# Kernel optimization log

Measured on AMD Instinct MI355X. Metric: run time of the kernel, lower is better.

The kernel has to match this reference:

```python
import jax, jax.numpy as jnp
import numpy as np

THRESHOLD = 1.0
SLOPE = 25.0  # snntorch surrogate.fast_sigmoid default slope
BETA = 0.9

@jax.custom_vjp
def spike_fn(x):
    # Heaviside forward, fast-sigmoid surrogate backward: g / (slope*|x| + 1)^2
    return (x > 0).astype(x.dtype)

def _spike_fwd(x):
    return spike_fn(x), x

def _spike_bwd(x, g):
    return (g / (SLOPE * jnp.abs(x) + 1.0) ** 2,)

spike_fn.defvjp(_spike_fwd, _spike_bwd)


def setup_inputs() -> dict:
    key = jax.random.key(0)
    k_x, k_w1, k_b1, k_w2, k_b2 = jax.random.split(key, 5)
    B, T, F, H, O = 128, 256, 2500, 128, 2
    x = jax.random.normal(k_x, (B, T, F), dtype=jnp.float32)
    # PyTorch Linear init: U(-1/sqrt(fan_in), 1/sqrt(fan_in))
    s1 = 1.0 / np.sqrt(F)
    s2 = 1.0 / np.sqrt(H)
    W1 = jax.random.uniform(k_w1, (H, F), jnp.float32, -s1, s1)
    b1 = jax.random.uniform(k_b1, (H,), jnp.float32, -s1, s1)
    W2 = jax.random.uniform(k_w2, (O, H), jnp.float32, -s2, s2)
    b2 = jax.random.uniform(k_b2, (O,), jnp.float32, -s2, s2)
    return {"x": x, "W1": W1, "b1": b1, "W2": W2, "b2": b2}


def reference(x, W1, b1, W2, b2):
    # Module transposes to [time, batch, feat] when shape[0] < shape[1]
    if x.ndim == 3 and x.shape[0] < x.shape[1]:
        x = jnp.swapaxes(x, 0, 1)  # [T, B, F]
    T, B = x.shape[0], x.shape[1]
    H, O = W1.shape[0], W2.shape[0]

    def lif(mem, cur):
        # snntorch Leaky, reset_mechanism='subtract'; reset spike is detached
        rst = jax.lax.stop_gradient(spike_fn(mem - THRESHOLD))
        mem = BETA * mem + cur - rst * THRESHOLD
        spk = spike_fn(mem - THRESHOLD)
        return spk, mem

    def step(carry, xt):
        mem1, mem2 = carry
        cur1 = xt @ W1.T + b1            # [B, H]
        spk1, mem1 = lif(mem1, cur1)
        cur2 = spk1 @ W2.T + b2          # [B, O]
        spk2, mem2 = lif(mem2, cur2)
        return (mem1, mem2), (spk2, mem2)

    mem1_0 = jnp.zeros((B, H), x.dtype)
    mem2_0 = jnp.zeros((B, O), x.dtype)
    _, (spk_rec, mem_rec) = jax.lax.scan(step, (mem1_0, mem2_0), x)
    return spk_rec, mem_rec  # each [T, B, O]
```

## Files before the change

kernel.cpp:

```cpp
#include <hip/hip_runtime.h>

#define T_STEPS 256
#define B_SZ    128
#define F_SZ    2500
#define H_SZ    128
#define O_SZ    2

__global__ __launch_bounds__(256) void k_transpose(const float* __restrict__ W1,
                                                   float* __restrict__ W1T) {
    int idx = blockIdx.x * 256 + threadIdx.x;
    if (idx >= F_SZ * H_SZ) return;
    int k = idx >> 7;
    int h = idx & 127;
    W1T[idx] = W1[h * F_SZ + k];
}

__global__ __launch_bounds__(256, 1) void k_gemm(const float* __restrict__ x,
                                                 const float* __restrict__ W1T,
                                                 const float* __restrict__ b1g,
                                                 double* __restrict__ cur1) {
    __shared__ float Alds[32 * 128];
    __shared__ float Blds[32 * 128];

    const int t    = blockIdx.x;
    const int tid  = threadIdx.x;
    const int lane = tid & 63;
    const int w    = tid >> 6;
    const int wm   = w >> 1;
    const int wn   = w & 1;
    const int li   = lane & 7;
    const int lj   = lane >> 3;

    const int ac = tid & 7;
    const int ar = tid >> 3;
    const int bn = tid & 31;
    const int bk = tid >> 5;

    float4 aV[4], bV[4];

    auto loadA = [&](int k0) {
        const int k = k0 + ac * 4;
        const bool ok = (k < F_SZ);
        #pragma unroll
        for (int i = 0; i < 4; ++i) {
            const int rr = ar + i * 32;
            if (ok) aV[i] = *(const float4*)(x + (size_t)(rr * T_STEPS + t) * F_SZ + k);
            else    aV[i] = make_float4(0.f, 0.f, 0.f, 0.f);
        }
    };
    auto loadB = [&](int k0) {
        #pragma unroll
        for (int i = 0; i < 4; ++i) {
            const int k = k0 + bk + i * 8;
            if (k < F_SZ) bV[i] = *(const float4*)(W1T + k * H_SZ + bn * 4);
            else          bV[i] = make_float4(0.f, 0.f, 0.f, 0.f);
        }
    };
    auto storeTiles = [&]() {
        #pragma unroll
        for (int i = 0; i < 4; ++i) {
            const int rr = ar + i * 32;
            Alds[(ac * 4 + 0) * 128 + rr] = aV[i].x;
            Alds[(ac * 4 + 1) * 128 + rr] = aV[i].y;
            Alds[(ac * 4 + 2) * 128 + rr] = aV[i].z;
            Alds[(ac * 4 + 3) * 128 + rr] = aV[i].w;
            *(float4*)(Blds + (bk + i * 8) * 128 + bn * 4) = bV[i];
        }
    };

    double acc[2][2][4][4];
    #pragma unroll
    for (int a = 0; a < 2; ++a)
        #pragma unroll
        for (int b = 0; b < 2; ++b)
            #pragma unroll
            for (int i = 0; i < 4; ++i)
                #pragma unroll
                for (int j = 0; j < 4; ++j)
                    acc[a][b][i][j] = 0.0;

    const int NSTEP = (F_SZ + 31) / 32;
    loadA(0);
    loadB(0);

    #pragma unroll 1
    for (int s = 0; s < NSTEP; ++s) {
        __syncthreads();
        storeTiles();
        if (s + 1 < NSTEP) { loadA((s + 1) * 32); loadB((s + 1) * 32); }
        __syncthreads();

        const float* Ab = Alds + wm * 64 + li * 4;
        const float* Bb = Blds + wn * 64 + lj * 4;
        #pragma unroll
        for (int k = 0; k < 32; ++k) {
            const float4 a0  = *(const float4*)(Ab + k * 128);
            const float4 a1  = *(const float4*)(Ab + k * 128 + 32);
            const float4 bb0 = *(const float4*)(Bb + k * 128);
            const float4 bb1 = *(const float4*)(Bb + k * 128 + 32);
            const double av[2][4] = {{a0.x, a0.y, a0.z, a0.w}, {a1.x, a1.y, a1.z, a1.w}};
            const double bv[2][4] = {{bb0.x, bb0.y, bb0.z, bb0.w}, {bb1.x, bb1.y, bb1.z, bb1.w}};
            #pragma unroll
            for (int rh = 0; rh < 2; ++rh)
                #pragma unroll
                for (int i = 0; i < 4; ++i)
                    #pragma unroll
                    for (int ch = 0; ch < 2; ++ch)
                        #pragma unroll
                        for (int j = 0; j < 4; ++j)
                            acc[rh][ch][i][j] = fma(av[rh][i], bv[ch][j], acc[rh][ch][i][j]);
        }
    }

    const float4 bias0 = *(const float4*)(b1g + wn * 64 + lj * 4);
    const float4 bias1 = *(const float4*)(b1g + wn * 64 + lj * 4 + 32);
    const double bias[2][4] = {{bias0.x, bias0.y, bias0.z, bias0.w},
                               {bias1.x, bias1.y, bias1.z, bias1.w}};
    #pragma unroll
    for (int rh = 0; rh < 2; ++rh) {
        #pragma unroll
        for (int i = 0; i < 4; ++i) {
            const int r = wm * 64 + li * 4 + rh * 32 + i;
            double* outp = cur1 + (size_t)(t * 128 + r) * 128 + wn * 64 + lj * 4;
            #pragma unroll
            for (int j = 0; j < 4; ++j) {
                outp[j]      = acc[rh][0][i][j] + bias[0][j];
                outp[j + 32] = acc[rh][1][i][j] + bias[1][j];
            }
        }
    }
}

__global__ __launch_bounds__(256) void k_lif1(const double* __restrict__ cur1,
                                              float* __restrict__ spk1) {
    const int tid = blockIdx.x * 256 + threadIdx.x;
    double mem = 0.0;
    #pragma unroll 4
    for (int t = 0; t < T_STEPS; ++t) {
        const double cur = cur1[t * 16384 + tid];
        const double rst = (mem > 1.0) ? 1.0 : 0.0;
        mem = 0.9 * mem + cur - rst;
        spk1[t * 16384 + tid] = (mem > 1.0) ? 1.0f : 0.0f;
    }
}

__global__ __launch_bounds__(256) void k_cur2(const float* __restrict__ spk1,
                                              const float* __restrict__ W2,
                                              const float* __restrict__ b2,
                                              double* __restrict__ cur2) {
    const int wave = (blockIdx.x * 256 + threadIdx.x) >> 6;
    const int lane = threadIdx.x & 63;
    const float2 s  = *(const float2*)(spk1 + (size_t)wave * 128 + lane * 2);
    const float2 w0 = *(const float2*)(W2 + lane * 2);
    const float2 w1 = *(const float2*)(W2 + 128 + lane * 2);
    double v0 = (double)s.x * (double)w0.x + (double)s.y * (double)w0.y;
    double v1 = (double)s.x * (double)w1.x + (double)s.y * (double)w1.y;
    #pragma unroll
    for (int off = 32; off >= 1; off >>= 1) {
        v0 += __shfl_down(v0, off);
        v1 += __shfl_down(v1, off);
    }
    if (lane == 0) {
        cur2[wave * 2 + 0] = v0 + (double)b2[0];
        cur2[wave * 2 + 1] = v1 + (double)b2[1];
    }
}

__global__ __launch_bounds__(256) void k_lif2(const double* __restrict__ cur2,
                                              float* __restrict__ out) {
    const int tid = threadIdx.x;
    double mem = 0.0;
    float* spk_out = out;
    float* mem_out = out + T_STEPS * B_SZ * O_SZ;
    #pragma unroll 4
    for (int t = 0; t < T_STEPS; ++t) {
        const double cur = cur2[t * 256 + tid];
        const double rst = (mem > 1.0) ? 1.0 : 0.0;
        mem = 0.9 * mem + cur - rst;
        spk_out[t * 256 + tid] = (mem > 1.0) ? 1.0f : 0.0f;
        mem_out[t * 256 + tid] = (float)mem;
    }
}

extern "C" void kernel_launch(void* const* d_in, const int* in_sizes, int n_in,
                              void* d_out, int out_size, void* d_ws, size_t ws_size,
                              hipStream_t stream) {
    const float* x  = (const float*)d_in[0];
    const float* W1 = (const float*)d_in[1];
    const float* b1 = (const float*)d_in[2];
    const float* W2 = (const float*)d_in[3];
    const float* b2 = (const float*)d_in[4];
    float* out = (float*)d_out;

    char* ws = (char*)d_ws;
    double* cur1 = (double*)ws;
    float*  spk1 = (float*)(ws + 33554432);
    float*  W1T  = (float*)(ws + 33554432 + 16777216);
    double* cur2 = (double*)(ws + 33554432 + 16777216 + 1280000);

    k_transpose<<<1250, 256, 0, stream>>>(W1, W1T);
    k_gemm<<<256, 256, 0, stream>>>(x, W1T, b1, cur1);
    k_lif1<<<64, 256, 0, stream>>>(cur1, spk1);
    k_cur2<<<8192, 256, 0, stream>>>(spk1, W2, b2, cur2);
    k_lif2<<<1, 256, 0, stream>>>(cur2, out);
}
```

Baseline: 923.1 us.

## Switch layer-1 GEMM to fp32 with split-K and double-precision fixup for near-threshold neurons

```diff
diff --git a/kernel.cpp b/kernel.cpp
--- a/kernel.cpp
+++ b/kernel.cpp
@@ -5,24 +5,36 @@
 #define F_SZ    2500
 #define H_SZ    128
 #define O_SZ    2
+#define KSPLIT0 1248
+#define FLAG_WINDOW 1.25e-4
+#define MAX_FLAGS 16384
 
 __global__ __launch_bounds__(256) void k_transpose(const float* __restrict__ W1,
-                                                   float* __restrict__ W1T) {
+                                                   float* __restrict__ W1T,
+                                                   int* __restrict__ flag_count) {
     int idx = blockIdx.x * 256 + threadIdx.x;
+    if (idx == 0) *flag_count = 0;
     if (idx >= F_SZ * H_SZ) return;
     int k = idx >> 7;
     int h = idx & 127;
     W1T[idx] = W1[h * F_SZ + k];
 }
 
-__global__ __launch_bounds__(256, 1) void k_gemm(const float* __restrict__ x,
+__global__ __launch_bounds__(256, 2) void k_gemm(const float* __restrict__ x,
                                                  const float* __restrict__ W1T,
-                                                 const float* __restrict__ b1g,
-                                                 double* __restrict__ cur1) {
-    __shared__ float Alds[32 * 128];
-    __shared__ float Blds[32 * 128];
-
-    const int t    = blockIdx.x;
+                                                 float* __restrict__ curA,
+                                                 float* __restrict__ curB) {
+    __shared__ float4 Alds4[128 * 8];
+    __shared__ float  Blds [32 * 128];
+
+    const int bid   = blockIdx.x;
+    const int t     = bid >> 1;
+    const int split = bid & 1;
+    const int k0    = split ? KSPLIT0 : 0;
+    const int kend  = split ? F_SZ : KSPLIT0;
+    const int NSTEP = split ? 40 : 39;
+    float* outP = split ? curB : curA;
+
     const int tid  = threadIdx.x;
     const int lane = tid & 63;
     const int w    = tid >> 6;
@@ -33,14 +45,15 @@
 
     const int ac = tid & 7;
     const int ar = tid >> 3;
+    const int aswz = ac ^ ((ar >> 2) & 7);
     const int bn = tid & 31;
     const int bk = tid >> 5;
 
     float4 aV[4], bV[4];
 
-    auto loadA = [&](int k0) {
-        const int k = k0 + ac * 4;
-        const bool ok = (k < F_SZ);
+    auto loadA = [&](int kb) {
+        const int k = kb + ac * 4;
+        const bool ok = (k < kend);
         #pragma unroll
         for (int i = 0; i < 4; ++i) {
             const int rr = ar + i * 32;
@@ -48,11 +61,11 @@
             else    aV[i] = make_float4(0.f, 0.f, 0.f, 0.f);
         }
     };
-    auto loadB = [&](int k0) {
+    auto loadB = [&](int kb) {
         #pragma unroll
         for (int i = 0; i < 4; ++i) {
-            const int k = k0 + bk + i * 8;
-            if (k < F_SZ) bV[i] = *(const float4*)(W1T + k * H_SZ + bn * 4);
+            const int k = kb + bk + i * 8;
+            if (k < kend) bV[i] = *(const float4*)(W1T + (size_t)k * H_SZ + bn * 4);
             else          bV[i] = make_float4(0.f, 0.f, 0.f, 0.f);
         }
     };
@@ -60,15 +73,12 @@
         #pragma unroll
         for (int i = 0; i < 4; ++i) {
             const int rr = ar + i * 32;
-            Alds[(ac * 4 + 0) * 128 + rr] = aV[i].x;
-            Alds[(ac * 4 + 1) * 128 + rr] = aV[i].y;
-            Alds[(ac * 4 + 2) * 128 + rr] = aV[i].z;
-            Alds[(ac * 4 + 3) * 128 + rr] = aV[i].w;
+            Alds4[rr * 8 + aswz] = aV[i];
             *(float4*)(Blds + (bk + i * 8) * 128 + bn * 4) = bV[i];
         }
     };
 
-    double acc[2][2][4][4];
+    float acc[2][2][4][4];
     #pragma unroll
     for (int a = 0; a < 2; ++a)
         #pragma unroll
@@ -77,70 +87,158 @@
             for (int i = 0; i < 4; ++i)
                 #pragma unroll
                 for (int j = 0; j < 4; ++j)
-                    acc[a][b][i][j] = 0.0;
-
-    const int NSTEP = (F_SZ + 31) / 32;
-    loadA(0);
-    loadB(0);
+                    acc[a][b][i][j] = 0.f;
+
+    int abase[8];
+    #pragma unroll
+    for (int rh = 0; rh < 2; ++rh)
+        #pragma unroll
+        for (int i = 0; i < 4; ++i)
+            abase[rh * 4 + i] = (wm * 64 + rh * 32 + li * 4 + i) * 8;
+
+    const float4* Blds4 = (const float4*)Blds;
+    const int bbase = wn * 16 + lj;
+
+    loadA(k0);
+    loadB(k0);
 
     #pragma unroll 1
     for (int s = 0; s < NSTEP; ++s) {
         __syncthreads();
         storeTiles();
-        if (s + 1 < NSTEP) { loadA((s + 1) * 32); loadB((s + 1) * 32); }
+        if (s + 1 < NSTEP) { loadA(k0 + (s + 1) * 32); loadB(k0 + (s + 1) * 32); }
         __syncthreads();
 
-        const float* Ab = Alds + wm * 64 + li * 4;
-        const float* Bb = Blds + wn * 64 + lj * 4;
-        #pragma unroll
-        for (int k = 0; k < 32; ++k) {
-            const float4 a0  = *(const float4*)(Ab + k * 128);
-            const float4 a1  = *(const float4*)(Ab + k * 128 + 32);
-            const float4 bb0 = *(const float4*)(Bb + k * 128);
-            const float4 bb1 = *(const float4*)(Bb + k * 128 + 32);
-            const double av[2][4] = {{a0.x, a0.y, a0.z, a0.w}, {a1.x, a1.y, a1.z, a1.w}};
-            const double bv[2][4] = {{bb0.x, bb0.y, bb0.z, bb0.w}, {bb1.x, bb1.y, bb1.z, bb1.w}};
-            #pragma unroll
-            for (int rh = 0; rh < 2; ++rh)
+        #pragma unroll
+        for (int kc = 0; kc < 8; ++kc) {
+            const int kcli = kc ^ li;
+            float4 av4[8];
+            #pragma unroll
+            for (int r = 0; r < 8; ++r) av4[r] = Alds4[abase[r] + kcli];
+
+            #pragma unroll
+            for (int dk = 0; dk < 4; ++dk) {
+                const float4 bv0 = Blds4[(kc * 4 + dk) * 32 + bbase];
+                const float4 bv1 = Blds4[(kc * 4 + dk) * 32 + bbase + 8];
+                const float bvf[2][4] = {{bv0.x, bv0.y, bv0.z, bv0.w},
+                                         {bv1.x, bv1.y, bv1.z, bv1.w}};
                 #pragma unroll
-                for (int i = 0; i < 4; ++i)
+                for (int rh = 0; rh < 2; ++rh)
                     #pragma unroll
-                    for (int ch = 0; ch < 2; ++ch)
+                    for (int i = 0; i < 4; ++i) {
+                        const float4 a4 = av4[rh * 4 + i];
+                        const float af = (dk == 0) ? a4.x : (dk == 1) ? a4.y : (dk == 2) ? a4.z : a4.w;
                         #pragma unroll
-                        for (int j = 0; j < 4; ++j)
-                            acc[rh][ch][i][j] = fma(av[rh][i], bv[ch][j], acc[rh][ch][i][j]);
-        }
-    }
-
-    const float4 bias0 = *(const float4*)(b1g + wn * 64 + lj * 4);
-    const float4 bias1 = *(const float4*)(b1g + wn * 64 + lj * 4 + 32);
-    const double bias[2][4] = {{bias0.x, bias0.y, bias0.z, bias0.w},
-                               {bias1.x, bias1.y, bias1.z, bias1.w}};
+                        for (int ch = 0; ch < 2; ++ch)
+                            #pragma unroll
+                            for (int j = 0; j < 4; ++j)
+                                acc[rh][ch][i][j] = fmaf(af, bvf[ch][j], acc[rh][ch][i][j]);
+                    }
+            }
+        }
+    }
+
     #pragma unroll
     for (int rh = 0; rh < 2; ++rh) {
         #pragma unroll
         for (int i = 0; i < 4; ++i) {
-            const int r = wm * 64 + li * 4 + rh * 32 + i;
-            double* outp = cur1 + (size_t)(t * 128 + r) * 128 + wn * 64 + lj * 4;
-            #pragma unroll
-            for (int j = 0; j < 4; ++j) {
-                outp[j]      = acc[rh][0][i][j] + bias[0][j];
-                outp[j + 32] = acc[rh][1][i][j] + bias[1][j];
-            }
-        }
-    }
-}
-
-__global__ __launch_bounds__(256) void k_lif1(const double* __restrict__ cur1,
-                                              float* __restrict__ spk1) {
-    const int tid = blockIdx.x * 256 + threadIdx.x;
+            const int r = wm * 64 + rh * 32 + li * 4 + i;
+            float* outp = outP + (size_t)(t * 128 + r) * 128 + wn * 64 + lj * 4;
+            *(float4*)(outp)      = make_float4(acc[rh][0][i][0], acc[rh][0][i][1],
+                                                acc[rh][0][i][2], acc[rh][0][i][3]);
+            *(float4*)(outp + 32) = make_float4(acc[rh][1][i][0], acc[rh][1][i][1],
+                                                acc[rh][1][i][2], acc[rh][1][i][3]);
+        }
+    }
+}
+
+__global__ __launch_bounds__(256) void k_lif1(const float* __restrict__ curA,
+                                              const float* __restrict__ curB,
+                                              const float* __restrict__ b1,
+                                              float* __restrict__ spk1,
+                                              int* __restrict__ flag_count,
+                                              int* __restrict__ flag_list) {
+    const int idx = blockIdx.x * 256 + threadIdx.x;
+    const double b1v = (double)b1[idx & 127];
     double mem = 0.0;
-    #pragma unroll 4
+    bool flagged = false;
+    #pragma unroll 8
     for (int t = 0; t < T_STEPS; ++t) {
-        const double cur = cur1[t * 16384 + tid];
+        const double cur = (double)curA[t * 16384 + idx] + (double)curB[t * 16384 + idx] + b1v;
         const double rst = (mem > 1.0) ? 1.0 : 0.0;
         mem = 0.9 * mem + cur - rst;
-        spk1[t * 16384 + tid] = (mem > 1.0) ? 1.0f : 0.0f;
+        spk1[t * 16384 + idx] = (mem > 1.0) ? 1.0f : 0.0f;
+        if (!flagged && fabs(mem - 1.0) < FLAG_WINDOW) {
+            flagged = true;
+            int p = atomicAdd(flag_count, 1);
+            if (p < MAX_FLAGS) flag_list[p] = idx;
+        }
+    }
+}
+
+__global__ __launch_bounds__(256) void k_fixup(const float* __restrict__ x,
+                                               const float* __restrict__ W1,
+                                               const float* __restrict__ b1,
+                                               float* __restrict__ spk1,
+                                               const int* __restrict__ flag_count,
+                                               const int* __restrict__ flag_list) {
+    const int gw   = (blockIdx.x * 256 + threadIdx.x) >> 6;
+    const int lane = threadIdx.x & 63;
+    int n = *flag_count;
+    if (n > MAX_FLAGS) n = MAX_FLAGS;
+
+    for (int i = gw; i < n; i += 512) {
+        const int idx = flag_list[i];
+        const int b = idx >> 7;
+        const int h = idx & 127;
+
+        float4 wv[10];
+        #pragma unroll
+        for (int j = 0; j < 10; ++j) {
+            const int wj = lane + 64 * j;
+            wv[j] = (wj < 625) ? ((const float4*)W1)[(size_t)h * 625 + wj]
+                               : make_float4(0.f, 0.f, 0.f, 0.f);
+        }
+        const float4* xb = (const float4*)x + (size_t)b * T_STEPS * 625;
+
+        float4 xv[10];
+        #pragma unroll
+        for (int j = 0; j < 10; ++j) {
+            const int wj = lane + 64 * j;
+            xv[j] = (wj < 625) ? xb[wj] : make_float4(0.f, 0.f, 0.f, 0.f);
+        }
+
+        double mem = 0.0;
+        const double b1v = (double)b1[h];
+        for (int t = 0; t < T_STEPS; ++t) {
+            float4 xn[10];
+            if (t + 1 < T_STEPS) {
+                #pragma unroll
+                for (int j = 0; j < 10; ++j) {
+                    const int wj = lane + 64 * j;
+                    xn[j] = (wj < 625) ? xb[(size_t)(t + 1) * 625 + wj]
+                                       : make_float4(0.f, 0.f, 0.f, 0.f);
+                }
+            }
+            double p = 0.0;
+            #pragma unroll
+            for (int j = 0; j < 10; ++j) {
+                p = fma((double)xv[j].x, (double)wv[j].x, p);
+                p = fma((double)xv[j].y, (double)wv[j].y, p);
+                p = fma((double)xv[j].z, (double)wv[j].z, p);
+                p = fma((double)xv[j].w, (double)wv[j].w, p);
+            }
+            #pragma unroll
+            for (int off = 32; off >= 1; off >>= 1) p += __shfl_down(p, off);
+            if (lane == 0) {
+                const double cur = p + b1v;
+                const double rst = (mem > 1.0) ? 1.0 : 0.0;
+                mem = 0.9 * mem + cur - rst;
+                spk1[t * 16384 + idx] = (mem > 1.0) ? 1.0f : 0.0f;
+            }
+            #pragma unroll
+            for (int j = 0; j < 10; ++j) xv[j] = xn[j];
+        }
     }
 }
 
@@ -172,7 +270,7 @@
     double mem = 0.0;
     float* spk_out = out;
     float* mem_out = out + T_STEPS * B_SZ * O_SZ;
-    #pragma unroll 4
+    #pragma unroll 8
     for (int t = 0; t < T_STEPS; ++t) {
         const double cur = cur2[t * 256 + tid];
         const double rst = (mem > 1.0) ? 1.0 : 0.0;
@@ -193,14 +291,18 @@
     float* out = (float*)d_out;
 
     char* ws = (char*)d_ws;
-    double* cur1 = (double*)ws;
+    float*  curA = (float*)ws;
+    float*  curB = (float*)(ws + 16777216);
     float*  spk1 = (float*)(ws + 33554432);
-    float*  W1T  = (float*)(ws + 33554432 + 16777216);
-    double* cur2 = (double*)(ws + 33554432 + 16777216 + 1280000);
-
-    k_transpose<<<1250, 256, 0, stream>>>(W1, W1T);
-    k_gemm<<<256, 256, 0, stream>>>(x, W1T, b1, cur1);
-    k_lif1<<<64, 256, 0, stream>>>(cur1, spk1);
+    float*  W1T  = (float*)(ws + 50331648);
+    double* cur2 = (double*)(ws + 50331648);
+    int*    flag_count = (int*)(ws + 51611648);
+    int*    flag_list  = (int*)(ws + 51611656);
+
+    k_transpose<<<1250, 256, 0, stream>>>(W1, W1T, flag_count);
+    k_gemm<<<512, 256, 0, stream>>>(x, W1T, curA, curB);
+    k_lif1<<<64, 256, 0, stream>>>(curA, curB, b1, spk1, flag_count, flag_list);
+    k_fixup<<<128, 256, 0, stream>>>(x, W1, b1, spk1, flag_count, flag_list);
     k_cur2<<<8192, 256, 0, stream>>>(spk1, W2, b2, cur2);
     k_lif2<<<1, 256, 0, stream>>>(cur2, out);
 }
```

Measured after the change: 1.278 ms. +38.4%, slower.

## Switch GEMM to fp32 with selective fp64 recompute for near-threshold neurons

Applied to the files above, without the earlier changes.

```diff
diff --git a/kernel.cpp b/kernel.cpp
--- a/kernel.cpp
+++ b/kernel.cpp
@@ -3,166 +3,251 @@
 #define T_STEPS 256
 #define B_SZ    128
 #define F_SZ    2500
+#define F4      625
 #define H_SZ    128
 #define O_SZ    2
+#define FLAG_WINDOW 5e-5
+#define CHUNK   12
 
 __global__ __launch_bounds__(256) void k_transpose(const float* __restrict__ W1,
-                                                   float* __restrict__ W1T) {
+                                                   float* __restrict__ W1T,
+                                                   int* __restrict__ nh) {
     int idx = blockIdx.x * 256 + threadIdx.x;
+    if (idx < B_SZ) nh[idx] = 0;
     if (idx >= F_SZ * H_SZ) return;
     int k = idx >> 7;
     int h = idx & 127;
     W1T[idx] = W1[h * F_SZ + k];
 }
 
-__global__ __launch_bounds__(256, 1) void k_gemm(const float* __restrict__ x,
+__global__ __launch_bounds__(256, 2) void k_gemm(const float* __restrict__ x,
                                                  const float* __restrict__ W1T,
-                                                 const float* __restrict__ b1g,
-                                                 double* __restrict__ cur1) {
-    __shared__ float Alds[32 * 128];
+                                                 float* __restrict__ cur1) {
+    __shared__ float Alds[32 * 64];
     __shared__ float Blds[32 * 128];
 
-    const int t    = blockIdx.x;
-    const int tid  = threadIdx.x;
-    const int lane = tid & 63;
-    const int w    = tid >> 6;
-    const int wm   = w >> 1;
-    const int wn   = w & 1;
-    const int li   = lane & 7;
-    const int lj   = lane >> 3;
+    const int t   = blockIdx.x >> 1;
+    const int b0  = (blockIdx.x & 1) * 64;
+    const int tid = threadIdx.x;
+    const int tc  = tid & 15;
+    const int tr  = tid >> 4;
 
     const int ac = tid & 7;
     const int ar = tid >> 3;
+    const int aswz = (ac & 3) << 3;
     const int bn = tid & 31;
     const int bk = tid >> 5;
 
-    float4 aV[4], bV[4];
-
-    auto loadA = [&](int k0) {
-        const int k = k0 + ac * 4;
+    float4 aV[2], bV[4];
+
+    auto loadA = [&](int kb) {
+        const int k = kb + ac * 4;
         const bool ok = (k < F_SZ);
+        const float* p0 = x + ((size_t)(b0 + ar) * T_STEPS + t) * F_SZ + k;
+        const float* p1 = x + ((size_t)(b0 + ar + 32) * T_STEPS + t) * F_SZ + k;
+        aV[0] = ok ? *(const float4*)p0 : make_float4(0.f, 0.f, 0.f, 0.f);
+        aV[1] = ok ? *(const float4*)p1 : make_float4(0.f, 0.f, 0.f, 0.f);
+    };
+    auto loadB = [&](int kb) {
         #pragma unroll
         for (int i = 0; i < 4; ++i) {
-            const int rr = ar + i * 32;
-            if (ok) aV[i] = *(const float4*)(x + (size_t)(rr * T_STEPS + t) * F_SZ + k);
-            else    aV[i] = make_float4(0.f, 0.f, 0.f, 0.f);
+            const int k = kb + bk + 8 * i;
+            bV[i] = (k < F_SZ) ? *(const float4*)(W1T + (size_t)k * H_SZ + bn * 4)
+                               : make_float4(0.f, 0.f, 0.f, 0.f);
         }
     };
-    auto loadB = [&](int k0) {
-        #pragma unroll
-        for (int i = 0; i < 4; ++i) {
-            const int k = k0 + bk + i * 8;
-            if (k < F_SZ) bV[i] = *(const float4*)(W1T + k * H_SZ + bn * 4);
-            else          bV[i] = make_float4(0.f, 0.f, 0.f, 0.f);
-        }
+    auto stage = [&]() {
+        const float* a0 = (const float*)&aV[0];
+        const float* a1 = (const float*)&aV[1];
+        #pragma unroll
+        for (int c = 0; c < 4; ++c) {
+            Alds[(ac * 4 + c) * 64 + (ar ^ aswz)]        = a0[c];
+            Alds[(ac * 4 + c) * 64 + ((ar + 32) ^ aswz)] = a1[c];
+        }
+        #pragma unroll
+        for (int i = 0; i < 4; ++i)
+            *(float4*)(Blds + (bk + 8 * i) * 128 + bn * 4) = bV[i];
     };
-    auto storeTiles = [&]() {
-        #pragma unroll
-        for (int i = 0; i < 4; ++i) {
-            const int rr = ar + i * 32;
-            Alds[(ac * 4 + 0) * 128 + rr] = aV[i].x;
-            Alds[(ac * 4 + 1) * 128 + rr] = aV[i].y;
-            Alds[(ac * 4 + 2) * 128 + rr] = aV[i].z;
-            Alds[(ac * 4 + 3) * 128 + rr] = aV[i].w;
-            *(float4*)(Blds + (bk + i * 8) * 128 + bn * 4) = bV[i];
-        }
-    };
-
-    double acc[2][2][4][4];
+
+    float acc0[4][4], acc1[4][4];
     #pragma unroll
-    for (int a = 0; a < 2; ++a)
-        #pragma unroll
-        for (int b = 0; b < 2; ++b)
+    for (int i = 0; i < 4; ++i)
+        #pragma unroll
+        for (int j = 0; j < 4; ++j) { acc0[i][j] = 0.f; acc1[i][j] = 0.f; }
+
+    const int NSTEP = 79;
+    loadA(0);
+    loadB(0);
+
+    #pragma unroll 1
+    for (int s = 0; s < NSTEP; ++s) {
+        __syncthreads();
+        stage();
+        if (s + 1 < NSTEP) { loadA((s + 1) * 32); loadB((s + 1) * 32); }
+        __syncthreads();
+
+        #pragma unroll
+        for (int k = 0; k < 32; ++k) {
+            const float4 a4  = *(const float4*)(Alds + k * 64 + ((tr * 4) ^ (((k >> 2) & 3) << 3)));
+            const float4 b4a = *(const float4*)(Blds + k * 128 + tc * 4);
+            const float4 b4b = *(const float4*)(Blds + k * 128 + 64 + tc * 4);
+            const float* af = (const float*)&a4;
+            const float* ba = (const float*)&b4a;
+            const float* bb = (const float*)&b4b;
             #pragma unroll
             for (int i = 0; i < 4; ++i)
                 #pragma unroll
-                for (int j = 0; j < 4; ++j)
-                    acc[a][b][i][j] = 0.0;
-
-    const int NSTEP = (F_SZ + 31) / 32;
-    loadA(0);
-    loadB(0);
-
-    #pragma unroll 1
-    for (int s = 0; s < NSTEP; ++s) {
-        __syncthreads();
-        storeTiles();
-        if (s + 1 < NSTEP) { loadA((s + 1) * 32); loadB((s + 1) * 32); }
-        __syncthreads();
-
-        const float* Ab = Alds + wm * 64 + li * 4;
-        const float* Bb = Blds + wn * 64 + lj * 4;
-        #pragma unroll
-        for (int k = 0; k < 32; ++k) {
-            const float4 a0  = *(const float4*)(Ab + k * 128);
-            const float4 a1  = *(const float4*)(Ab + k * 128 + 32);
-            const float4 bb0 = *(const float4*)(Bb + k * 128);
-            const float4 bb1 = *(const float4*)(Bb + k * 128 + 32);
-            const double av[2][4] = {{a0.x, a0.y, a0.z, a0.w}, {a1.x, a1.y, a1.z, a1.w}};
-            const double bv[2][4] = {{bb0.x, bb0.y, bb0.z, bb0.w}, {bb1.x, bb1.y, bb1.z, bb1.w}};
-            #pragma unroll
-            for (int rh = 0; rh < 2; ++rh)
-                #pragma unroll
-                for (int i = 0; i < 4; ++i)
-                    #pragma unroll
-                    for (int ch = 0; ch < 2; ++ch)
-                        #pragma unroll
-                        for (int j = 0; j < 4; ++j)
-                            acc[rh][ch][i][j] = fma(av[rh][i], bv[ch][j], acc[rh][ch][i][j]);
-        }
-    }
-
-    const float4 bias0 = *(const float4*)(b1g + wn * 64 + lj * 4);
-    const float4 bias1 = *(const float4*)(b1g + wn * 64 + lj * 4 + 32);
-    const double bias[2][4] = {{bias0.x, bias0.y, bias0.z, bias0.w},
-                               {bias1.x, bias1.y, bias1.z, bias1.w}};
+                for (int j = 0; j < 4; ++j) {
+                    acc0[i][j] = fmaf(af[i], ba[j], acc0[i][j]);
+                    acc1[i][j] = fmaf(af[i], bb[j], acc1[i][j]);
+                }
+        }
+    }
+
     #pragma unroll
-    for (int rh = 0; rh < 2; ++rh) {
-        #pragma unroll
-        for (int i = 0; i < 4; ++i) {
-            const int r = wm * 64 + li * 4 + rh * 32 + i;
-            double* outp = cur1 + (size_t)(t * 128 + r) * 128 + wn * 64 + lj * 4;
-            #pragma unroll
-            for (int j = 0; j < 4; ++j) {
-                outp[j]      = acc[rh][0][i][j] + bias[0][j];
-                outp[j + 32] = acc[rh][1][i][j] + bias[1][j];
-            }
-        }
-    }
-}
-
-__global__ __launch_bounds__(256) void k_lif1(const double* __restrict__ cur1,
-                                              float* __restrict__ spk1) {
-    const int tid = blockIdx.x * 256 + threadIdx.x;
+    for (int i = 0; i < 4; ++i) {
+        const int bg = b0 + tr * 4 + i;
+        float* op = cur1 + ((size_t)t * B_SZ + bg) * H_SZ + tc * 4;
+        *(float4*)op        = make_float4(acc0[i][0], acc0[i][1], acc0[i][2], acc0[i][3]);
+        *(float4*)(op + 64) = make_float4(acc1[i][0], acc1[i][1], acc1[i][2], acc1[i][3]);
+    }
+}
+
+__global__ __launch_bounds__(256) void k_lif1(const float* __restrict__ cur1,
+                                              const float* __restrict__ b1,
+                                              unsigned long long* __restrict__ spk_bits,
+                                              int* __restrict__ nh,
+                                              int* __restrict__ hlist) {
+    const int idx = blockIdx.x * 256 + threadIdx.x;
+    const int b = idx >> 7, h = idx & 127;
+    const double b1v = (double)b1[h];
     double mem = 0.0;
-    #pragma unroll 4
+    bool flagged = false;
     for (int t = 0; t < T_STEPS; ++t) {
-        const double cur = cur1[t * 16384 + tid];
+        const double cur = (double)cur1[(size_t)t * 16384 + idx] + b1v;
         const double rst = (mem > 1.0) ? 1.0 : 0.0;
-        mem = 0.9 * mem + cur - rst;
-        spk1[t * 16384 + tid] = (mem > 1.0) ? 1.0f : 0.0f;
-    }
-}
-
-__global__ __launch_bounds__(256) void k_cur2(const float* __restrict__ spk1,
+        mem = fma(0.9, mem, cur) - rst;
+        const bool spk = (mem > 1.0);
+        const unsigned long long m = __ballot(spk);
+        if ((threadIdx.x & 63) == 0)
+            spk_bits[((size_t)t * B_SZ + b) * 2 + ((h >> 6) & 1)] = m;
+        if (!flagged && fabs(mem - 1.0) < FLAG_WINDOW) {
+            flagged = true;
+            int s = atomicAdd(&nh[b], 1);
+            hlist[b * 128 + s] = h;
+        }
+    }
+}
+
+__global__ __launch_bounds__(256) void k_cur2(const unsigned long long* __restrict__ bits,
                                               const float* __restrict__ W2,
                                               const float* __restrict__ b2,
                                               double* __restrict__ cur2) {
-    const int wave = (blockIdx.x * 256 + threadIdx.x) >> 6;
-    const int lane = threadIdx.x & 63;
-    const float2 s  = *(const float2*)(spk1 + (size_t)wave * 128 + lane * 2);
-    const float2 w0 = *(const float2*)(W2 + lane * 2);
-    const float2 w1 = *(const float2*)(W2 + 128 + lane * 2);
-    double v0 = (double)s.x * (double)w0.x + (double)s.y * (double)w0.y;
-    double v1 = (double)s.x * (double)w1.x + (double)s.y * (double)w1.y;
-    #pragma unroll
-    for (int off = 32; off >= 1; off >>= 1) {
-        v0 += __shfl_down(v0, off);
-        v1 += __shfl_down(v1, off);
-    }
-    if (lane == 0) {
-        cur2[wave * 2 + 0] = v0 + (double)b2[0];
-        cur2[wave * 2 + 1] = v1 + (double)b2[1];
+    __shared__ float w2s[256];
+    w2s[threadIdx.x] = W2[threadIdx.x];
+    __syncthreads();
+    const int pair = blockIdx.x * 256 + threadIdx.x;
+    unsigned long long m0 = bits[(size_t)pair * 2];
+    unsigned long long m1 = bits[(size_t)pair * 2 + 1];
+    double v0 = (double)b2[0], v1 = (double)b2[1];
+    while (m0) {
+        const int i = __ffsll((long long)m0) - 1; m0 &= m0 - 1;
+        v0 += (double)w2s[i]; v1 += (double)w2s[128 + i];
+    }
+    while (m1) {
+        const int i = __ffsll((long long)m1) - 1; m1 &= m1 - 1;
+        v0 += (double)w2s[64 + i]; v1 += (double)w2s[192 + i];
+    }
+    cur2[(size_t)pair * 2]     = v0;
+    cur2[(size_t)pair * 2 + 1] = v1;
+}
+
+__global__ __launch_bounds__(256) void k_fixA(const float* __restrict__ x,
+                                              const float* __restrict__ W1,
+                                              const int* __restrict__ nh,
+                                              const int* __restrict__ hlist,
+                                              double* __restrict__ cur_fix) {
+    const int b   = blockIdx.x >> 4;
+    const int tch = blockIdx.x & 15;
+    const int n   = nh[b];
+    if (n == 0) return;
+
+    __shared__ float w1s[CHUNK * F_SZ];
+    const int tid  = threadIdx.x;
+    const int wv   = tid >> 6;
+    const int lane = tid & 63;
+
+    for (int c0 = 0; c0 < n; c0 += CHUNK) {
+        const int nc = (n - c0 < CHUNK) ? (n - c0) : CHUNK;
+        __syncthreads();
+        for (int r = 0; r < nc; ++r) {
+            const int h = hlist[b * 128 + c0 + r];
+            const float4* src = (const float4*)W1 + (size_t)h * F4;
+            float4* dst = (float4*)(w1s + r * F_SZ);
+            for (int c = tid; c < F4; c += 256) dst[c] = src[c];
+        }
+        __syncthreads();
+
+        #pragma unroll 1
+        for (int tt = 0; tt < 4; ++tt) {
+            const int t = tch * 16 + wv * 4 + tt;
+            float4 xv[10];
+            const float4* xb = (const float4*)x + ((size_t)b * T_STEPS + t) * F4;
+            #pragma unroll
+            for (int j = 0; j < 10; ++j) {
+                const int c = lane + 64 * j;
+                xv[j] = (c < F4) ? xb[c] : make_float4(0.f, 0.f, 0.f, 0.f);
+            }
+            for (int s = 0; s < nc; ++s) {
+                const float* wr = w1s + s * F_SZ;
+                double p = 0.0;
+                #pragma unroll
+                for (int j = 0; j < 10; ++j) {
+                    const int c = lane + 64 * j;
+                    if (c < F4) {
+                        const float4 w4 = *(const float4*)(wr + c * 4);
+                        p = fma((double)xv[j].x, (double)w4.x, p);
+                        p = fma((double)xv[j].y, (double)w4.y, p);
+                        p = fma((double)xv[j].z, (double)w4.z, p);
+                        p = fma((double)xv[j].w, (double)w4.w, p);
+                    }
+                }
+                #pragma unroll
+                for (int off = 32; off >= 1; off >>= 1) p += __shfl_down(p, off);
+                if (lane == 0)
+                    cur_fix[((size_t)b * 128 + c0 + s) * T_STEPS + t] = p;
+            }
+        }
+    }
+}
+
+__global__ __launch_bounds__(128) void k_fixB(const float* __restrict__ cur1,
+                                              const double* __restrict__ cur_fix,
+                                              const float* __restrict__ b1,
+                                              const float* __restrict__ W2,
+                                              const int* __restrict__ nh,
+                                              const int* __restrict__ hlist,
+                                              double* __restrict__ cur2) {
+    const int b = blockIdx.x;
+    const int s = threadIdx.x;
+    if (s >= nh[b]) return;
+    const int h = hlist[b * 128 + s];
+    const double b1v = (double)b1[h];
+    const double w0 = (double)W2[h], w1 = (double)W2[128 + h];
+    double ma = 0.0, me = 0.0;
+    for (int t = 0; t < T_STEPS; ++t) {
+        const double ca = (double)cur1[((size_t)t * B_SZ + b) * H_SZ + h] + b1v;
+        const double ce = cur_fix[((size_t)b * 128 + s) * T_STEPS + t] + b1v;
+        const double ra = (ma > 1.0) ? 1.0 : 0.0;
+        const double re = (me > 1.0) ? 1.0 : 0.0;
+        ma = fma(0.9, ma, ca) - ra;
+        me = fma(0.9, me, ce) - re;
+        const bool sa = (ma > 1.0), se = (me > 1.0);
+        if (sa != se) {
+            const double d = se ? 1.0 : -1.0;
+            atomicAdd(&cur2[((size_t)t * B_SZ + b) * 2 + 0], d * w0);
+            atomicAdd(&cur2[((size_t)t * B_SZ + b) * 2 + 1], d * w1);
+        }
     }
 }
 
@@ -172,11 +257,11 @@
     double mem = 0.0;
     float* spk_out = out;
     float* mem_out = out + T_STEPS * B_SZ * O_SZ;
-    #pragma unroll 4
+    #pragma unroll 8
     for (int t = 0; t < T_STEPS; ++t) {
         const double cur = cur2[t * 256 + tid];
         const double rst = (mem > 1.0) ? 1.0 : 0.0;
-        mem = 0.9 * mem + cur - rst;
+        mem = fma(0.9, mem, cur) - rst;
         spk_out[t * 256 + tid] = (mem > 1.0) ? 1.0f : 0.0f;
         mem_out[t * 256 + tid] = (float)mem;
     }
@@ -193,14 +278,19 @@
     float* out = (float*)d_out;
 
     char* ws = (char*)d_ws;
-    double* cur1 = (double*)ws;
-    float*  spk1 = (float*)(ws + 33554432);
-    float*  W1T  = (float*)(ws + 33554432 + 16777216);
-    double* cur2 = (double*)(ws + 33554432 + 16777216 + 1280000);
-
-    k_transpose<<<1250, 256, 0, stream>>>(W1, W1T);
-    k_gemm<<<256, 256, 0, stream>>>(x, W1T, b1, cur1);
-    k_lif1<<<64, 256, 0, stream>>>(cur1, spk1);
-    k_cur2<<<8192, 256, 0, stream>>>(spk1, W2, b2, cur2);
+    float*  cur1     = (float*)ws;
+    float*  W1T      = (float*)(ws + 16777216);
+    double* cur2     = (double*)(ws + 18057216);
+    double* cur_fix  = (double*)(ws + 18581504);
+    int*    nh       = (int*)(ws + 52135936);
+    int*    hlist    = (int*)(ws + 52136448);
+    unsigned long long* spk_bits = (unsigned long long*)(ws + 52201984);
+
+    k_transpose<<<1250, 256, 0, stream>>>(W1, W1T, nh);
+    k_gemm<<<512, 256, 0, stream>>>(x, W1T, cur1);
+    k_lif1<<<64, 256, 0, stream>>>(cur1, b1, spk_bits, nh, hlist);
+    k_cur2<<<128, 256, 0, stream>>>(spk_bits, W2, b2, cur2);
+    k_fixA<<<2048, 256, 0, stream>>>(x, W1, nh, hlist, cur_fix);
+    k_fixB<<<128, 128, 0, stream>>>(cur1, cur_fix, b1, W2, nh, hlist, cur2);
     k_lif2<<<1, 256, 0, stream>>>(cur2, out);
 }
```

After: 827.5 us. 1.12x faster.
